# Kernel tuning notes

Hardware: AMD Instinct MI355X
Metric: run time of the kernel (lower is better)

The kernel has to match this reference:

```python
import jax, jax.numpy as jnp
import numpy as np

B, S, D_IN, D_OUT = 4, 2048, 1024, 1024


def setup_inputs() -> dict:
    key = jax.random.key(0)
    ks = jax.random.split(key, 6)
    scale = 1.0 / np.sqrt(D_IN)
    return {
        "inputs_for_keys": jax.random.normal(ks[0], (B, S, D_IN), jnp.float32),
        "inputs_for_values": jax.random.normal(ks[1], (B, S, D_IN), jnp.float32),
        "inputs_for_queries": jax.random.normal(ks[2], (B, S, D_IN), jnp.float32),
        "WK": jax.random.uniform(ks[3], (D_IN, D_OUT), jnp.float32, -scale, scale),
        "WQ": jax.random.uniform(ks[4], (D_IN, D_OUT), jnp.float32, -scale, scale),
        "WV": jax.random.uniform(ks[5], (D_IN, D_OUT), jnp.float32, -scale, scale),
    }


def reference(inputs_for_keys, inputs_for_values, inputs_for_queries, WK, WQ, WV):
    # QKV projections: [B,S,Din] @ [Din,Dout] -> [B,S,Dout]
    keys = jnp.einsum("bsd,de->bse", inputs_for_keys, WK)
    values = jnp.einsum("bsd,de->bse", inputs_for_values, WV)
    queries = jnp.einsum("bsd,de->bse", inputs_for_queries, WQ)
    d_k = keys.shape[-1]
    # scaled scores [B,S,S]
    scores = jnp.einsum("bqe,bke->bqk", queries, keys) / jnp.sqrt(jnp.float32(d_k))
    # causal mask: position k > q gets -inf (strictly upper triangular)
    q_idx = jnp.arange(S)[:, None]
    k_idx = jnp.arange(S)[None, :]
    scores = jnp.where(k_idx > q_idx, -jnp.inf, scores)
    att = jax.nn.softmax(scores, axis=-1)
    out = jnp.einsum("bqk,bke->bqe", att, values)  # [B,S,Dout]
    return out
```

## Files before the change

### kernel.cpp

```cpp
#include <hip/hip_runtime.h>
#include <stdint.h>


typedef __attribute__((ext_vector_type(8))) short short8;
typedef __attribute__((ext_vector_type(8))) unsigned short ushort8;
typedef __attribute__((ext_vector_type(4))) unsigned short ushort4v;
typedef __attribute__((ext_vector_type(4))) float f32x4;

__device__ __forceinline__ unsigned short f2bf(float f) {
  union { float f; unsigned u; } v; v.f = f;
  unsigned u = v.u + 0x7FFFu + ((v.u >> 16) & 1u);
  return (unsigned short)(u >> 16);
}
__device__ __forceinline__ float bf2f(unsigned short h) {
  union { unsigned u; float f; } v; v.u = ((unsigned)h) << 16;
  return v.f;
}

__device__ __forceinline__ void gload16(const void* g, void* l) {
  __builtin_amdgcn_global_load_lds(
      (const __attribute__((address_space(1))) unsigned int*)g,
      (__attribute__((address_space(3))) unsigned int*)l, 16, 0, 0);
}

template<int N> __device__ __forceinline__ void vmwait() {
  static_assert(N >= 0 && N <= 8, "vmcnt range");
  if constexpr (N == 0) asm volatile("s_waitcnt vmcnt(0)" ::: "memory");
  else if constexpr (N == 1) asm volatile("s_waitcnt vmcnt(1)" ::: "memory");
  else if constexpr (N == 2) asm volatile("s_waitcnt vmcnt(2)" ::: "memory");
  else if constexpr (N == 3) asm volatile("s_waitcnt vmcnt(3)" ::: "memory");
  else if constexpr (N == 4) asm volatile("s_waitcnt vmcnt(4)" ::: "memory");
  else if constexpr (N == 5) asm volatile("s_waitcnt vmcnt(5)" ::: "memory");
  else if constexpr (N == 6) asm volatile("s_waitcnt vmcnt(6)" ::: "memory");
  else if constexpr (N == 7) asm volatile("s_waitcnt vmcnt(7)" ::: "memory");
  else asm volatile("s_waitcnt vmcnt(8)" ::: "memory");
}
__device__ __forceinline__ void barrier_() { asm volatile("s_barrier" ::: "memory"); }
__device__ __forceinline__ void lgkm0() { asm volatile("s_waitcnt lgkmcnt(0)" ::: "memory"); }

__device__ __forceinline__ void cvt_tail(const float* __restrict__ in,
                                         unsigned short* __restrict__ out,
                                         int bx, int nblk, int tid) {
  for (int c = bx; c < 2048; c += nblk) {
    const long i = (long)c * 4096 + tid * 8;
    float4 a = *(const float4*)(in + i);
    float4 b = *(const float4*)(in + i + 4);
    ushort8 r;
    r[0] = f2bf(a.x); r[1] = f2bf(a.y); r[2] = f2bf(a.z); r[3] = f2bf(a.w);
    r[4] = f2bf(b.x); r[5] = f2bf(b.y); r[6] = f2bf(b.z); r[7] = f2bf(b.w);
    *(ushort8*)(out + i) = r;
  }
}

__global__ __launch_bounds__(256)
void prep(const float* __restrict__ Xv, unsigned short* __restrict__ Ov,
          const float* __restrict__ WQ, const float* __restrict__ WK,
          const float* __restrict__ WV,
          unsigned short* __restrict__ WQb, unsigned short* __restrict__ WKb,
          unsigned short* __restrict__ WVT) {
  const int bx = blockIdx.x;
  const int tid = threadIdx.x;
  if (bx < 1024) {
    const long base = (long)bx * 8192;
    float4 v[8];
#pragma unroll
    for (int j = 0; j < 8; ++j)
      v[j] = *(const float4*)(Xv + base + j * 1024 + tid * 4);
#pragma unroll
    for (int j = 0; j < 8; ++j) {
      ushort4v r;
      r[0] = f2bf(v[j].x); r[1] = f2bf(v[j].y);
      r[2] = f2bf(v[j].z); r[3] = f2bf(v[j].w);
      *(ushort4v*)(Ov + base + j * 1024 + tid * 4) = r;
    }
  } else if (bx < 1280) {
    const int wi = bx - 1024;
    const float* in = wi < 128 ? WQ : WK;
    unsigned short* out = wi < 128 ? WQb : WKb;
    const float s = wi < 128 ? 0.03125f : 1.0f;
    const long base = (long)(wi & 127) * 8192;
    float4 v[8];
#pragma unroll
    for (int j = 0; j < 8; ++j)
      v[j] = *(const float4*)(in + base + j * 1024 + tid * 4);
#pragma unroll
    for (int j = 0; j < 8; ++j) {
      ushort4v r;
      r[0] = f2bf(v[j].x * s); r[1] = f2bf(v[j].y * s);
      r[2] = f2bf(v[j].z * s); r[3] = f2bf(v[j].w * s);
      *(ushort4v*)(out + base + j * 1024 + tid * 4) = r;
    }
  } else {
    const int rem = bx - 1280;
    __shared__ float tbuf[32][33];
    const int bk = (rem >> 5) * 32, be = (rem & 31) * 32;
    const int tx = tid & 31, ty = tid >> 5;
#pragma unroll
    for (int j = 0; j < 32; j += 8)
      tbuf[ty + j][tx] = WV[(long)(bk + ty + j) * 1024 + (be + tx)];
    __syncthreads();
#pragma unroll
    for (int j = 0; j < 32; j += 8)
      WVT[(long)(be + ty + j) * 1024 + (bk + tx)] = f2bf(tbuf[tx][ty + j]);
  }
}

template<typename CT, int MF, int NF>
__device__ __forceinline__ void gemm_body(const unsigned short* __restrict__ A,
                                          const unsigned short* __restrict__ B,
                                          CT* __restrict__ C,
                                          int bm, int bn, int kmax,
                                          int lda, int ldb, int ldc,
                                          char* AL, char* BL) {
  constexpr int BM = MF * 32, BN = NF * 64;
  constexpr int LA = BM / 128, LB = BN / 128;
  constexpr int S = 2 * (LA + LB);

  const int tid = threadIdx.x;
  const int lane = tid & 63, wid = tid >> 6;
  const int wr = wid >> 2, wc = wid & 3;
  const int fr = lane & 15, fq = lane >> 4;
  const int srow = tid >> 2;
  const int scol = (((tid & 3) ^ ((tid >> 3) & 3)) << 3);
  const int m0 = bm * BM, n0 = bn * BN;
  const int nt = kmax >> 6;

  f32x4 acc[MF][NF] = {};

  const unsigned short* As = A + (long)(m0 + srow) * lda + scol;
  const unsigned short* Bs = B + (long)(n0 + srow) * ldb + scol;

  auto stageTile = [&](int b, int kt) {
#pragma unroll
    for (int h = 0; h < 2; ++h) {
#pragma unroll
      for (int l = 0; l < LA; ++l)
        gload16(As + (long)l * 128 * lda + kt * 64 + h * 32,
                AL + b * (BM * 128) + h * (BM * 64) + l * 8192 + tid * 16);
#pragma unroll
      for (int l = 0; l < LB; ++l)
        gload16(Bs + (long)l * 128 * ldb + kt * 64 + h * 32,
                BL + b * (BN * 128) + h * (BN * 64) + l * 8192 + tid * 16);
    }
  };

  const int aoff = (wr * (BM / 2) + fr) * 64 + ((fq ^ ((fr >> 1) & 3)) << 4);
  const int boff = (wc * (BN / 4) + fr) * 64 + ((fq ^ ((fr >> 1) & 3)) << 4);
  auto ardf = [&](int b, int kk, int m) -> short8 {
    return *(const short8*)(AL + b * (BM * 128) + kk * (BM * 64) + aoff + m * 1024);
  };
  auto brdf = [&](int b, int kk, int n) -> short8 {
    return *(const short8*)(BL + b * (BN * 128) + kk * (BN * 64) + boff + n * 1024);
  };

  stageTile(0, 0);

  for (int u = 0; u < nt; ++u) {
    const int cb = u & 1, nb = cb ^ 1;
    lgkm0();
    barrier_();
    if (u + 1 < nt) { stageTile(nb, u + 1); vmwait<S>(); }
    else            { vmwait<0>(); }
    barrier_();
#pragma unroll
    for (int kk = 0; kk < 2; ++kk) {
      short8 bfr[NF], af[MF / 2];
#pragma unroll
      for (int n = 0; n < NF; ++n) bfr[n] = brdf(cb, kk, n);
#pragma unroll
      for (int m = 0; m < MF / 2; ++m) af[m] = ardf(cb, kk, m);
      __builtin_amdgcn_s_setprio(1);
#pragma unroll
      for (int m = 0; m < MF / 2; ++m)
#pragma unroll
        for (int n = 0; n < NF; ++n)
          acc[m][n] = __builtin_amdgcn_mfma_f32_16x16x32_bf16(af[m], bfr[n], acc[m][n], 0, 0, 0);
      __builtin_amdgcn_s_setprio(0);
#pragma unroll
      for (int m = 0; m < MF / 2; ++m) af[m] = ardf(cb, kk, MF / 2 + m);
      __builtin_amdgcn_s_setprio(1);
#pragma unroll
      for (int m = 0; m < MF / 2; ++m)
#pragma unroll
        for (int n = 0; n < NF; ++n)
          acc[MF / 2 + m][n] =
              __builtin_amdgcn_mfma_f32_16x16x32_bf16(af[m], bfr[n], acc[MF / 2 + m][n], 0, 0, 0);
      __builtin_amdgcn_s_setprio(0);
    }
  }

#pragma unroll
  for (int m = 0; m < MF; ++m) {
    const int row = m0 + wr * (BM / 2) + m * 16 + fq * 4;
#pragma unroll
    for (int n = 0; n < NF; ++n) {
      const int col = n0 + wc * (BN / 4) + n * 16 + fr;
#pragma unroll
      for (int r = 0; r < 4; ++r) {
        float v = acc[m][n][r];
        if constexpr (sizeof(CT) == 2)
          C[(long)(row + r) * ldc + col] = (CT)f2bf(v);
        else
          C[(long)(row + r) * ldc + col] = (CT)v;
      }
    }
  }
}

__global__ __launch_bounds__(512, 2)
void d2_gemm(const unsigned short* __restrict__ WVT, const unsigned short* __restrict__ Xvb,
             unsigned short* __restrict__ VT,
             const unsigned short* __restrict__ WKb, const unsigned short* __restrict__ WQb,
             unsigned short* __restrict__ Mt,
             const float* __restrict__ Xq, unsigned short* __restrict__ Xqb) {
  __shared__ __align__(16) char pool[65536];
  const int id = (blockIdx.x & 7) * 72 + (blockIdx.x >> 3);
  if (id < 512)
    gemm_body<unsigned short, 4, 2>(WVT, Xvb, VT, id >> 6, id & 63, 1024,
                                    1024, 1024, 8192, pool, pool + 32768);
  else {
    const int t = id - 512;
    gemm_body<unsigned short, 4, 2>(WKb, WQb, Mt, t >> 3, t & 7, 1024,
                                    1024, 1024, 1024, pool, pool + 32768);
  }
  cvt_tail(Xq, Xqb, blockIdx.x, 576, threadIdx.x);
}

__global__ __launch_bounds__(512, 2)
void y_gemm(const unsigned short* __restrict__ Xqb, const unsigned short* __restrict__ Mt,
            unsigned short* __restrict__ Y,
            const float* __restrict__ Xk, unsigned short* __restrict__ Xkb) {
  __shared__ __align__(16) char pool[65536];
  const int id = (blockIdx.x & 7) * 64 + (blockIdx.x >> 3);
  gemm_body<unsigned short, 4, 2>(Xqb, Mt, Y, id >> 3, id & 7, 1024,
                                  1024, 1024, 1024, pool, pool + 32768);
  cvt_tail(Xk, Xkb, blockIdx.x, 512, threadIdx.x);
}

__global__ __launch_bounds__(512, 4)
void scores_gemm(const unsigned short* __restrict__ Y, const unsigned short* __restrict__ Xkb,
                 unsigned short* __restrict__ S) {
  __shared__ __align__(16) char pool[65536];
  const int gid = (blockIdx.x & 7) * 68 + (blockIdx.x >> 3);
  const int bz = gid / 136, t = gid - bz * 136;
  int bm = (int)((__fsqrt_rn(8.0f * t + 1.0f) - 1.0f) * 0.5f);
  while ((bm + 1) * (bm + 2) / 2 <= t) ++bm;
  while (bm * (bm + 1) / 2 > t) --bm;
  const int bn = t - bm * (bm + 1) / 2;
  gemm_body<unsigned short, 4, 2>(Y + (long)bz * 2048 * 1024, Xkb + (long)bz * 2048 * 1024,
                                  S + (long)bz * 2048 * 2048, bm, bn, 1024,
                                  1024, 1024, 2048, pool, pool + 32768);
}

__global__ __launch_bounds__(512, 4)
void pv_gemm(const unsigned short* __restrict__ P, const unsigned short* __restrict__ VT,
             float* __restrict__ O) {
  __shared__ __align__(16) char pool[65536];
  const int b = blockIdx.x;
  int bm, r;
  if (b < 256) { bm = 15 - (b >> 5); r = b & 31; }
  else         { bm = (b - 256) >> 5; r = b & 31; }
  const int bn = r & 7, bz = r >> 3;
  gemm_body<float, 4, 2>(P + (long)bz * 2048 * 2048, VT + (long)bz * 2048,
                         O + (long)bz * 2048 * 1024, bm, bn, (bm + 1) * 128,
                         2048, 8192, 1024, pool, pool + 32768);
}

__global__ __launch_bounds__(256)
void softmax_causal(unsigned short* __restrict__ P) {
  const int row = blockIdx.x;
  const int q = row & 2047;
  unsigned short* p = P + (long)row * 2048;
  const int nfill = ((q >> 7) + 1) << 7;
  const int tid = threadIdx.x;
  const int lane = tid & 63, wid = tid >> 6;
  const int i0 = tid * 8;
  __shared__ float red[8];

  float v[8];
  float lmax = -3.0e38f;
  if (i0 <= q) {
    ushort8 v8 = *(const ushort8*)(p + i0);
#pragma unroll
    for (int j = 0; j < 8; ++j) {
      float f = bf2f(v8[j]);
      f = (i0 + j <= q) ? f : -3.0e38f;
      v[j] = f;
      lmax = fmaxf(lmax, f);
    }
  } else {
#pragma unroll
    for (int j = 0; j < 8; ++j) v[j] = -3.0e38f;
  }
#pragma unroll
  for (int off = 1; off < 64; off <<= 1)
    lmax = fmaxf(lmax, __shfl_xor(lmax, off));
  if (lane == 0) red[wid] = lmax;
  __syncthreads();
  const float mx = fmaxf(fmaxf(red[0], red[1]), fmaxf(red[2], red[3]));

  float lsum = 0.f;
#pragma unroll
  for (int j = 0; j < 8; ++j) {
    float e = __expf(v[j] - mx);
    v[j] = e;
    lsum += e;
  }
#pragma unroll
  for (int off = 1; off < 64; off <<= 1)
    lsum += __shfl_xor(lsum, off);
  if (lane == 0) red[4 + wid] = lsum;
  __syncthreads();
  const float inv = 1.0f / (red[4] + red[5] + red[6] + red[7]);

  if (i0 < nfill) {
    ushort8 r;
#pragma unroll
    for (int j = 0; j < 8; ++j)
      r[j] = (i0 + j <= q) ? f2bf(v[j] * inv) : (unsigned short)0;
    *(ushort8*)(p + i0) = r;
  }
}

extern "C" void kernel_launch(void* const* d_in, const int* in_sizes, int n_in,
                              void* d_out, int out_size, void* d_ws, size_t ws_size,
                              hipStream_t stream) {
  const float* Xk = (const float*)d_in[0];
  const float* Xv = (const float*)d_in[1];
  const float* Xq = (const float*)d_in[2];
  const float* WK = (const float*)d_in[3];
  const float* WQ = (const float*)d_in[4];
  const float* WV = (const float*)d_in[5];
  float* out = (float*)d_out;

  unsigned short* ws = (unsigned short*)d_ws;
  const long NE = 8L * 1024 * 1024;
  unsigned short* Xkb = ws + 0 * NE;
  unsigned short* Xqb = ws + 1 * NE;
  unsigned short* Xvb = ws + 2 * NE;
  unsigned short* Yb  = ws + 3 * NE;
  unsigned short* VTb = ws + 4 * NE;
  unsigned short* WQb = ws + 5 * NE;
  unsigned short* WKb = WQb + 1024 * 1024;
  unsigned short* WVT = WKb + 1024 * 1024;
  unsigned short* Mtb = WVT + 1024 * 1024;
  unsigned short* Sc  = ws + 1 * NE;

  dim3 b256(256), b512(512);
  prep<<<2304, b256, 0, stream>>>(Xv, Xvb, WQ, WK, WV, WQb, WKb, WVT);
  d2_gemm<<<576, b512, 0, stream>>>(WVT, Xvb, VTb, WKb, WQb, Mtb, Xq, Xqb);
  y_gemm<<<512, b512, 0, stream>>>(Xqb, Mtb, Yb, Xk, Xkb);
  scores_gemm<<<544, b512, 0, stream>>>(Yb, Xkb, Sc);
  softmax_causal<<<8192, b256, 0, stream>>>(Sc);
  pv_gemm<<<512, b512, 0, stream>>>(Sc, VTb, out);
}
```

Measured before the change: 146.8 us.

## Move Xq/Xk bf16 conversion into dedicated blocks of d2_gemm

The fp32-to-bf16 conversions of Xq and Xk used to run as tails after the GEMM work in d2_gemm and y_gemm. They now run in 128 dedicated blocks at the start of the d2_gemm grid, each converting a contiguous slice, so that the conversions overlap with the GEMM blocks instead of lengthening every block. y_gemm no longer carries a tail, and its launch bound is raised to 4 blocks per CU. The risk is that the extra blocks add a partial wave to d2_gemm, and that the occupancy hint may force register limits on y_gemm.

```diff
diff --git a/kernel.cpp b/kernel.cpp
--- a/kernel.cpp
+++ b/kernel.cpp
@@ -38,17 +38,22 @@
 __device__ __forceinline__ void barrier_() { asm volatile("s_barrier" ::: "memory"); }
 __device__ __forceinline__ void lgkm0() { asm volatile("s_waitcnt lgkmcnt(0)" ::: "memory"); }
 
-__device__ __forceinline__ void cvt_tail(const float* __restrict__ in,
-                                         unsigned short* __restrict__ out,
-                                         int bx, int nblk, int tid) {
-  for (int c = bx; c < 2048; c += nblk) {
-    const long i = (long)c * 4096 + tid * 8;
+__device__ __forceinline__ void cvt_slice(const float* __restrict__ in,
+                                          unsigned short* __restrict__ out,
+                                          long base, int tid) {
+  for (int j = 0; j < 16; ++j) {
+    const long i = base + (long)j * 8192 + tid * 8;
     float4 a = *(const float4*)(in + i);
     float4 b = *(const float4*)(in + i + 4);
-    ushort8 r;
-    r[0] = f2bf(a.x); r[1] = f2bf(a.y); r[2] = f2bf(a.z); r[3] = f2bf(a.w);
-    r[4] = f2bf(b.x); r[5] = f2bf(b.y); r[6] = f2bf(b.z); r[7] = f2bf(b.w);
-    *(ushort8*)(out + i) = r;
+    float4 c = *(const float4*)(in + i + 4096);
+    float4 d = *(const float4*)(in + i + 4100);
+    ushort8 r0, r1;
+    r0[0] = f2bf(a.x); r0[1] = f2bf(a.y); r0[2] = f2bf(a.z); r0[3] = f2bf(a.w);
+    r0[4] = f2bf(b.x); r0[5] = f2bf(b.y); r0[6] = f2bf(b.z); r0[7] = f2bf(b.w);
+    r1[0] = f2bf(c.x); r1[1] = f2bf(c.y); r1[2] = f2bf(c.z); r1[3] = f2bf(c.w);
+    r1[4] = f2bf(d.x); r1[5] = f2bf(d.y); r1[6] = f2bf(d.z); r1[7] = f2bf(d.w);
+    *(ushort8*)(out + i) = r0;
+    *(ushort8*)(out + i + 4096) = r1;
   }
 }
 
@@ -212,9 +217,18 @@
              unsigned short* __restrict__ VT,
              const unsigned short* __restrict__ WKb, const unsigned short* __restrict__ WQb,
              unsigned short* __restrict__ Mt,
-             const float* __restrict__ Xq, unsigned short* __restrict__ Xqb) {
+             const float* __restrict__ Xq, unsigned short* __restrict__ Xqb,
+             const float* __restrict__ Xk, unsigned short* __restrict__ Xkb) {
   __shared__ __align__(16) char pool[65536];
-  const int id = (blockIdx.x & 7) * 72 + (blockIdx.x >> 3);
+  const int bx = blockIdx.x;
+  if (bx < 128) {
+    const float* in = bx < 64 ? Xq : Xk;
+    unsigned short* out = bx < 64 ? Xqb : Xkb;
+    cvt_slice(in, out, (long)(bx & 63) * 131072, threadIdx.x);
+    return;
+  }
+  const int g = bx - 128;
+  const int id = (g & 7) * 72 + (g >> 3);
   if (id < 512)
     gemm_body<unsigned short, 4, 2>(WVT, Xvb, VT, id >> 6, id & 63, 1024,
                                     1024, 1024, 8192, pool, pool + 32768);
@@ -223,18 +237,15 @@
     gemm_body<unsigned short, 4, 2>(WKb, WQb, Mt, t >> 3, t & 7, 1024,
                                     1024, 1024, 1024, pool, pool + 32768);
   }
-  cvt_tail(Xq, Xqb, blockIdx.x, 576, threadIdx.x);
-}
-
-__global__ __launch_bounds__(512, 2)
+}
+
+__global__ __launch_bounds__(512, 4)
 void y_gemm(const unsigned short* __restrict__ Xqb, const unsigned short* __restrict__ Mt,
-            unsigned short* __restrict__ Y,
-            const float* __restrict__ Xk, unsigned short* __restrict__ Xkb) {
+            unsigned short* __restrict__ Y) {
   __shared__ __align__(16) char pool[65536];
   const int id = (blockIdx.x & 7) * 64 + (blockIdx.x >> 3);
   gemm_body<unsigned short, 4, 2>(Xqb, Mt, Y, id >> 3, id & 7, 1024,
                                   1024, 1024, 1024, pool, pool + 32768);
-  cvt_tail(Xk, Xkb, blockIdx.x, 512, threadIdx.x);
 }
 
 __global__ __launch_bounds__(512, 4)
@@ -348,8 +359,9 @@
 
   dim3 b256(256), b512(512);
   prep<<<2304, b256, 0, stream>>>(Xv, Xvb, WQ, WK, WV, WQb, WKb, WVT);
-  d2_gemm<<<576, b512, 0, stream>>>(WVT, Xvb, VTb, WKb, WQb, Mtb, Xq, Xqb);
-  y_gemm<<<512, b512, 0, stream>>>(Xqb, Mtb, Yb, Xk, Xkb);
+  d2_gemm<<<704, b512, 0, stream>>>(WVT, Xvb, VTb, WKb, WQb, Mtb,
+                                    Xq, Xqb, Xk, Xkb);
+  y_gemm<<<512, b512, 0, stream>>>(Xqb, Mtb, Yb);
   scores_gemm<<<544, b512, 0, stream>>>(Yb, Xkb, Sc);
   softmax_causal<<<8192, b256, 0, stream>>>(Sc);
   pv_gemm<<<512, b512, 0, stream>>>(Sc, VTb, out);
```

Measured after the change: 144.1 us. Within noise of the previous version (-1.8%).
